# Optimization experiments

Measured on AMD Instinct MI355X. Metric: run time of the kernel, lower is better.

## Reference

```python
import jax, jax.numpy as jnp
import numpy as np
from jax import lax

STRIDE = 1
PAD = 1  # module pads 1 on each side whenever padding != 0


def setup_inputs() -> dict:
    key = jax.random.key(0)
    kx, kw, kb = jax.random.split(key, 3)
    x = jax.random.normal(kx, (4096, 4096), dtype=jnp.float32)
    weight = jax.random.normal(kw, (15, 15), dtype=jnp.float32)
    bias = jax.random.normal(kb, (1,), dtype=jnp.float32)
    return {"x": x, "weight": weight, "bias": bias}


def reference(x, weight, bias):
    # Single-channel 2D cross-correlation with constant zero padding of 1 and
    # stride STRIDE, plus a scalar bias. lax.conv_general_dilated computes
    # correlation (no kernel flip), matching the torch corr2d loop exactly.
    out = lax.conv_general_dilated(
        x[None, None, :, :],          # NCHW, N=C=1
        weight[None, None, :, :],      # OIHW, O=I=1
        window_strides=(STRIDE, STRIDE),
        padding=[(PAD, PAD), (PAD, PAD)],
        dimension_numbers=("NCHW", "OIHW", "NCHW"),
    )[0, 0]
    return out + bias[0]
```

## Files before the change

### kernel.cpp

```cpp
#include <hip/hip_runtime.h>

#define IN_N   4096
#define OW     4084
#define KS     15
#define TILE   64
#define XROWS  78
#define XCOLS  80
#define XS     88
#define NBX    64
#define NBY    64

typedef __attribute__((ext_vector_type(8))) short v8s;
typedef __attribute__((ext_vector_type(4))) float v4f;

__device__ __forceinline__ unsigned short f2bf(float f) {
    union { float f; unsigned u; } c; c.f = f;
    unsigned r = c.u + 0x7fff + ((c.u >> 16) & 1);
    return (unsigned short)(r >> 16);
}

__global__ void build_B(const float* __restrict__ w, unsigned short* __restrict__ Bg) {
    int ky = blockIdx.x;
    int e  = threadIdx.x;
    int n = e & 15, quad = e >> 4;
    unsigned short vals[8];
    #pragma unroll
    for (int j = 0; j < 8; ++j) {
        int d = quad * 8 + j - n;
        vals[j] = (d >= 0 && d < KS) ? f2bf(w[ky * KS + d]) : (unsigned short)0;
    }
    *(v8s*)(&Bg[(ky * 64 + e) * 8]) = *(const v8s*)vals;
}

__global__ __launch_bounds__(256, 6) void conv2d_mfma2(
    const float* __restrict__ x, const unsigned short* __restrict__ Bg,
    const float* __restrict__ bias, float* __restrict__ out)
{
    __shared__ unsigned short xtile[XROWS * XS] __attribute__((aligned(16)));

    const int tid = threadIdx.x;
    const int bx = blockIdx.x, by = blockIdx.y;
    const int X0 = bx * TILE;
    const int Y0 = by * TILE;

    const int tx = tid % 40;
    const int ty = tid / 40;
    const bool interior = (bx > 0) & (bx < NBX - 1) & (by > 0) & (by < NBY - 1);

    if (ty < 6) {
        unsigned short* dst = &xtile[ty * XS + 2 * tx];
        if (interior) {
            const float* xr = x + (size_t)(Y0 - 1 + ty) * IN_N + (X0 - 1 + 2 * tx);
            #pragma unroll
            for (int i = 0; i < 13; ++i) {
                float f0 = xr[0], f1 = xr[1];
                *(unsigned*)dst = (unsigned)f2bf(f0) | ((unsigned)f2bf(f1) << 16);
                xr  += 6 * IN_N;
                dst += 6 * XS;
            }
        } else {
            const int gc0 = X0 - 1 + 2 * tx;
            #pragma unroll
            for (int i = 0; i < 13; ++i) {
                int gr = Y0 - 1 + ty + 6 * i;
                float f0 = 0.0f, f1 = 0.0f;
                if ((unsigned)gr < (unsigned)IN_N) {
                    const float* xr = x + (size_t)gr * IN_N;
                    if ((unsigned)gc0       < (unsigned)IN_N) f0 = xr[gc0];
                    if ((unsigned)(gc0 + 1) < (unsigned)IN_N) f1 = xr[gc0 + 1];
                }
                *(unsigned*)dst = (unsigned)f2bf(f0) | ((unsigned)f2bf(f1) << 16);
                dst += 6 * XS;
            }
        }
    }
    __syncthreads();

    const int lane = tid & 63;
    const int wv   = tid >> 6;
    const int m    = lane & 15;
    const int quad = lane >> 4;

    v4f acc[4];
    #pragma unroll
    for (int t = 0; t < 4; ++t) acc[t] = (v4f){0.f, 0.f, 0.f, 0.f};

    const v8s* Bgv = (const v8s*)Bg;
    v8s bcur = Bgv[lane];
    const unsigned short* arow = &xtile[(wv * 16 + m) * XS + quad * 8];

    #pragma unroll
    for (int ky = 0; ky < KS; ++ky) {
        v8s bnext = (ky < KS - 1) ? Bgv[(ky + 1) * 64 + lane] : bcur;
        v8s a0 = *(const v8s*)(arow + 0);
        v8s a1 = *(const v8s*)(arow + 16);
        v8s a2 = *(const v8s*)(arow + 32);
        v8s a3 = *(const v8s*)(arow + 48);
        acc[0] = __builtin_amdgcn_mfma_f32_16x16x32_bf16(a0, bcur, acc[0], 0, 0, 0);
        acc[1] = __builtin_amdgcn_mfma_f32_16x16x32_bf16(a1, bcur, acc[1], 0, 0, 0);
        acc[2] = __builtin_amdgcn_mfma_f32_16x16x32_bf16(a2, bcur, acc[2], 0, 0, 0);
        acc[3] = __builtin_amdgcn_mfma_f32_16x16x32_bf16(a3, bcur, acc[3], 0, 0, 0);
        arow += XS;
        bcur = bnext;
    }

    const float bv = bias[0];
    const int orow0 = Y0 + wv * 16 + quad * 4;
    const int ocol0 = X0 + m;
    if (interior | ((bx < NBX - 1) & (by < NBY - 1))) {
        float* o0 = &out[(size_t)orow0 * OW + ocol0];
        #pragma unroll
        for (int t = 0; t < 4; ++t) {
            #pragma unroll
            for (int r = 0; r < 4; ++r)
                o0[(size_t)r * OW + t * 16] = acc[t][r] + bv;
        }
    } else {
        #pragma unroll
        for (int t = 0; t < 4; ++t) {
            int oc = ocol0 + t * 16;
            if (oc < OW) {
                #pragma unroll
                for (int r = 0; r < 4; ++r) {
                    int orow = orow0 + r;
                    if (orow < OW)
                        out[(size_t)orow * OW + oc] = acc[t][r] + bv;
                }
            }
        }
    }
}

extern "C" void kernel_launch(void* const* d_in, const int* in_sizes, int n_in,
                              void* d_out, int out_size, void* d_ws, size_t ws_size,
                              hipStream_t stream) {
    const float* x    = (const float*)d_in[0];
    const float* w    = (const float*)d_in[1];
    const float* bias = (const float*)d_in[2];
    float* out        = (float*)d_out;
    unsigned short* Bg = (unsigned short*)d_ws;

    build_B<<<dim3(KS), dim3(64), 0, stream>>>(w, Bg);
    dim3 grid(NBX, NBY);
    conv2d_mfma2<<<grid, dim3(256), 0, stream>>>(x, Bg, bias, out);
}
```

Baseline: 136.4 us.

## Process four tiles per block with register-prefetched double-buffered LDS staging

Each block now walks four horizontally adjacent 64x64 output tiles instead of one. While the MFMA loop runs on the current tile, the global loads for the next tile are issued into registers; they are packed to bf16 and written into a second LDS buffer after the compute. The aim is to hide global-load latency behind matrix work and to spread per-block setup over more output. In exchange the grid shrinks to a quarter of the blocks and occupancy is capped at 4 blocks per CU, which reduces latency hiding through parallelism.

```diff
diff --git a/kernel.cpp b/kernel.cpp
--- a/kernel.cpp
+++ b/kernel.cpp
@@ -5,10 +5,10 @@
 #define KS     15
 #define TILE   64
 #define XROWS  78
-#define XCOLS  80
 #define XS     88
-#define NBX    64
+#define NBXT   64
 #define NBY    64
+#define TPB    4
 
 typedef __attribute__((ext_vector_type(8))) short v8s;
 typedef __attribute__((ext_vector_type(4))) float v4f;
@@ -18,10 +18,12 @@
     unsigned r = c.u + 0x7fff + ((c.u >> 16) & 1);
     return (unsigned short)(r >> 16);
 }
+__device__ __forceinline__ unsigned pack2(float a, float b) {
+    return (unsigned)f2bf(a) | ((unsigned)f2bf(b) << 16);
+}
 
 __global__ void build_B(const float* __restrict__ w, unsigned short* __restrict__ Bg) {
-    int ky = blockIdx.x;
-    int e  = threadIdx.x;
+    int ky = blockIdx.x, e = threadIdx.x;
     int n = e & 15, quad = e >> 4;
     unsigned short vals[8];
     #pragma unroll
@@ -32,31 +34,38 @@
     *(v8s*)(&Bg[(ky * 64 + e) * 8]) = *(const v8s*)vals;
 }
 
-__global__ __launch_bounds__(256, 6) void conv2d_mfma2(
+__global__ __launch_bounds__(256, 4) void conv2d_mfma3(
     const float* __restrict__ x, const unsigned short* __restrict__ Bg,
     const float* __restrict__ bias, float* __restrict__ out)
 {
-    __shared__ unsigned short xtile[XROWS * XS] __attribute__((aligned(16)));
+    __shared__ unsigned short buf[2][XROWS * XS] __attribute__((aligned(16)));
 
     const int tid = threadIdx.x;
-    const int bx = blockIdx.x, by = blockIdx.y;
-    const int X0 = bx * TILE;
-    const int Y0 = by * TILE;
+    const int gbx = blockIdx.x, by = blockIdx.y;
+    const int Y0  = by * TILE;
+    const int bx0 = gbx * TPB;
 
     const int tx = tid % 40;
     const int ty = tid / 40;
-    const bool interior = (bx > 0) & (bx < NBX - 1) & (by > 0) & (by < NBY - 1);
+    const bool act = (ty < 6);
 
-    if (ty < 6) {
-        unsigned short* dst = &xtile[ty * XS + 2 * tx];
-        if (interior) {
+    const int lane = tid & 63, wv = tid >> 6;
+    const int m = lane & 15, quad = lane >> 4;
+    const v8s* Bgv = (const v8s*)Bg;
+    const float bv = bias[0];
+
+    float pf0[13], pf1[13];
+
+    auto load_tile = [&](int bx) {
+        if (!act) return;
+        const int X0 = bx * TILE;
+        const bool fast = (bx > 0) & (bx < NBXT - 1) & (by > 0) & (by < NBY - 1);
+        if (fast) {
             const float* xr = x + (size_t)(Y0 - 1 + ty) * IN_N + (X0 - 1 + 2 * tx);
             #pragma unroll
             for (int i = 0; i < 13; ++i) {
-                float f0 = xr[0], f1 = xr[1];
-                *(unsigned*)dst = (unsigned)f2bf(f0) | ((unsigned)f2bf(f1) << 16);
-                xr  += 6 * IN_N;
-                dst += 6 * XS;
+                pf0[i] = xr[0]; pf1[i] = xr[1];
+                xr += 6 * (size_t)IN_N;
             }
         } else {
             const int gc0 = X0 - 1 + 2 * tx;
@@ -69,64 +78,80 @@
                     if ((unsigned)gc0       < (unsigned)IN_N) f0 = xr[gc0];
                     if ((unsigned)(gc0 + 1) < (unsigned)IN_N) f1 = xr[gc0 + 1];
                 }
-                *(unsigned*)dst = (unsigned)f2bf(f0) | ((unsigned)f2bf(f1) << 16);
-                dst += 6 * XS;
+                pf0[i] = f0; pf1[i] = f1;
             }
         }
-    }
+    };
+
+    auto store_tile = [&](unsigned short* b) {
+        if (!act) return;
+        unsigned* dst = (unsigned*)&b[ty * XS + 2 * tx];
+        #pragma unroll
+        for (int i = 0; i < 13; ++i) {
+            *dst = pack2(pf0[i], pf1[i]);
+            dst += 3 * XS;
+        }
+    };
+
+    load_tile(bx0);
+    store_tile(buf[0]);
     __syncthreads();
 
-    const int lane = tid & 63;
-    const int wv   = tid >> 6;
-    const int m    = lane & 15;
-    const int quad = lane >> 4;
+    #pragma unroll
+    for (int j = 0; j < TPB; ++j) {
+        const int bx = bx0 + j;
+        const int X0 = bx * TILE;
 
-    v4f acc[4];
-    #pragma unroll
-    for (int t = 0; t < 4; ++t) acc[t] = (v4f){0.f, 0.f, 0.f, 0.f};
+        if (j < TPB - 1) load_tile(bx + 1);
 
-    const v8s* Bgv = (const v8s*)Bg;
-    v8s bcur = Bgv[lane];
-    const unsigned short* arow = &xtile[(wv * 16 + m) * XS + quad * 8];
+        v4f acc[4];
+        #pragma unroll
+        for (int t = 0; t < 4; ++t) acc[t] = (v4f){0.f, 0.f, 0.f, 0.f};
 
-    #pragma unroll
-    for (int ky = 0; ky < KS; ++ky) {
-        v8s bnext = (ky < KS - 1) ? Bgv[(ky + 1) * 64 + lane] : bcur;
-        v8s a0 = *(const v8s*)(arow + 0);
-        v8s a1 = *(const v8s*)(arow + 16);
-        v8s a2 = *(const v8s*)(arow + 32);
-        v8s a3 = *(const v8s*)(arow + 48);
-        acc[0] = __builtin_amdgcn_mfma_f32_16x16x32_bf16(a0, bcur, acc[0], 0, 0, 0);
-        acc[1] = __builtin_amdgcn_mfma_f32_16x16x32_bf16(a1, bcur, acc[1], 0, 0, 0);
-        acc[2] = __builtin_amdgcn_mfma_f32_16x16x32_bf16(a2, bcur, acc[2], 0, 0, 0);
-        acc[3] = __builtin_amdgcn_mfma_f32_16x16x32_bf16(a3, bcur, acc[3], 0, 0, 0);
-        arow += XS;
-        bcur = bnext;
-    }
+        const unsigned short* arow = &buf[j & 1][(wv * 16 + m) * XS + quad * 8];
+        v8s bcur = Bgv[lane];
+        #pragma unroll
+        for (int ky = 0; ky < KS; ++ky) {
+            v8s bnext = (ky < KS - 1) ? Bgv[(ky + 1) * 64 + lane] : bcur;
+            v8s a0 = *(const v8s*)(arow + 0);
+            v8s a1 = *(const v8s*)(arow + 16);
+            v8s a2 = *(const v8s*)(arow + 32);
+            v8s a3 = *(const v8s*)(arow + 48);
+            acc[0] = __builtin_amdgcn_mfma_f32_16x16x32_bf16(a0, bcur, acc[0], 0, 0, 0);
+            acc[1] = __builtin_amdgcn_mfma_f32_16x16x32_bf16(a1, bcur, acc[1], 0, 0, 0);
+            acc[2] = __builtin_amdgcn_mfma_f32_16x16x32_bf16(a2, bcur, acc[2], 0, 0, 0);
+            acc[3] = __builtin_amdgcn_mfma_f32_16x16x32_bf16(a3, bcur, acc[3], 0, 0, 0);
+            arow += XS;
+            bcur = bnext;
+        }
 
-    const float bv = bias[0];
-    const int orow0 = Y0 + wv * 16 + quad * 4;
-    const int ocol0 = X0 + m;
-    if (interior | ((bx < NBX - 1) & (by < NBY - 1))) {
-        float* o0 = &out[(size_t)orow0 * OW + ocol0];
-        #pragma unroll
-        for (int t = 0; t < 4; ++t) {
+        const int orow0 = Y0 + wv * 16 + quad * 4;
+        const int ocol0 = X0 + m;
+        if ((bx < NBXT - 1) & (by < NBY - 1)) {
+            float* o0 = &out[(size_t)orow0 * OW + ocol0];
             #pragma unroll
-            for (int r = 0; r < 4; ++r)
-                o0[(size_t)r * OW + t * 16] = acc[t][r] + bv;
-        }
-    } else {
-        #pragma unroll
-        for (int t = 0; t < 4; ++t) {
-            int oc = ocol0 + t * 16;
-            if (oc < OW) {
+            for (int t = 0; t < 4; ++t)
                 #pragma unroll
-                for (int r = 0; r < 4; ++r) {
-                    int orow = orow0 + r;
-                    if (orow < OW)
-                        out[(size_t)orow * OW + oc] = acc[t][r] + bv;
+                for (int r = 0; r < 4; ++r)
+                    o0[(size_t)r * OW + t * 16] = acc[t][r] + bv;
+        } else {
+            #pragma unroll
+            for (int t = 0; t < 4; ++t) {
+                int oc = ocol0 + t * 16;
+                if (oc < OW) {
+                    #pragma unroll
+                    for (int r = 0; r < 4; ++r) {
+                        int orow = orow0 + r;
+                        if (orow < OW)
+                            out[(size_t)orow * OW + oc] = acc[t][r] + bv;
+                    }
                 }
             }
+        }
+
+        if (j < TPB - 1) {
+            store_tile(&buf[(j + 1) & 1][0]);
+            __syncthreads();
         }
     }
 }
@@ -141,6 +166,6 @@
     unsigned short* Bg = (unsigned short*)d_ws;
 
     build_B<<<dim3(KS), dim3(64), 0, stream>>>(w, Bg);
-    dim3 grid(NBX, NBY);
-    conv2d_mfma2<<<grid, dim3(256), 0, stream>>>(x, Bg, bias, out);
+    dim3 grid(NBXT / TPB, NBY);
+    conv2d_mfma3<<<grid, dim3(256), 0, stream>>>(x, Bg, bias, out);
 }
```

Measured after the change: 137.3 us. Within noise of the previous version (+0.6%).
